# Optimization experiments

Measured on AMD Instinct MI355X. Metric: run time of the kernel, lower is better.

The kernel has to match this reference:

```python
import jax, jax.numpy as jnp
import numpy as np

C = 512
H = 8

def setup_inputs() -> dict:
    key = jax.random.key(0)
    ks = jax.random.split(key, 5)
    x = jax.random.normal(ks[0], (4, C, 2048), dtype=jnp.float32)
    # Conv1d(kernel_size=1) == pointwise linear: weight [out, in], bias [out]
    qkv_w = jax.random.normal(ks[1], (3 * C, C), dtype=jnp.float32) * (1.0 / np.sqrt(C))
    qkv_b = jax.random.normal(ks[2], (3 * C,), dtype=jnp.float32) * 0.02
    proj_w = jax.random.normal(ks[3], (C, C), dtype=jnp.float32) * (1.0 / np.sqrt(C))
    proj_b = jax.random.normal(ks[4], (C,), dtype=jnp.float32) * 0.02
    return {"x": x, "qkv_w": qkv_w, "qkv_b": qkv_b, "proj_w": proj_w, "proj_b": proj_b}

def reference(x, qkv_w, qkv_b, proj_w, proj_b):
    b, c, t = x.shape
    scale = c ** (-0.5)  # NOTE: full channel count, matching the torch module
    # pointwise conv: [3C, C] @ [b, C, T] -> [b, 3C, T]
    qkv = jnp.einsum('oc,bct->bot', qkv_w, x) + qkv_b[None, :, None]
    q, k, v = jnp.split(qkv, 3, axis=1)
    d = c // H
    q = q.reshape(b, H, d, t)
    k = k.reshape(b, H, d, t)
    v = v.reshape(b, H, d, t)
    attn = jnp.einsum('bhct,bhcs->bhts', q, k) * scale
    attn = jax.nn.softmax(attn, axis=-1)
    out = jnp.einsum('bhts,bhcs->bhct', attn, v)
    out = out.reshape(b, c, t)
    out = jnp.einsum('oc,bct->bot', proj_w, out) + proj_b[None, :, None]
    return x + out
```

## Files before the change

kernel.cpp:

```cpp
#include <hip/hip_runtime.h>
#include <hip/hip_bf16.h>
#include <math.h>

#define B_DIM 4
#define C_DIM 512
#define T_DIM 2048
#define H_DIM 8
#define OC3   1536
#define VN_STRIDE 2064
#define SCALE 0.044194173824159216f
#define SCALE2 (0.044194173824159216f * 1.4426950408889634f)

typedef unsigned short ushortT;
typedef unsigned int uintT;
typedef __attribute__((ext_vector_type(8))) short bf16x8;
typedef __attribute__((ext_vector_type(4))) short bf16x4;
typedef __attribute__((ext_vector_type(4))) float f32x4;

__device__ __forceinline__ ushortT f2bf(float f) {
    union { float f; uintT u; } v; v.f = f;
    uintT r = v.u + 0x7FFF + ((v.u >> 16) & 1);
    return (ushortT)(r >> 16);
}
__device__ __forceinline__ float bf2f(ushortT h) {
    union { uintT u; float f; } v; v.u = ((uintT)h) << 16;
    return v.f;
}
__device__ __forceinline__ uintT pack2bf(float a, float b) {
    uintT ua = __float_as_uint(a) + 0x8000u;
    uintT ub = __float_as_uint(b) + 0x8000u;
    return (ua >> 16) | (ub & 0xFFFF0000u);
}
__device__ __forceinline__ uintT cvtpk2bf(float a, float b) {
    union { __bf16 v[2]; uintT u; } c;
    c.v[0] = (__bf16)a; c.v[1] = (__bf16)b;
    return c.u;
}
__device__ __forceinline__ void gload_lds16(const ushortT* g, ushortT* l) {
    __builtin_amdgcn_global_load_lds(
        (const __attribute__((address_space(1))) void*)g,
        (__attribute__((address_space(3))) void*)l, 16, 0, 0);
}

__global__ __launch_bounds__(256) void prep(const float* __restrict__ x,
                                            const float* __restrict__ qw,
                                            const float* __restrict__ pw,
                                            ushortT* __restrict__ xb,
                                            ushortT* __restrict__ qwb,
                                            ushortT* __restrict__ pwb) {
    __shared__ float xs[64][65];
    const int tid = threadIdx.x;
    const int blk = blockIdx.x;
    if (blk >= 1024) {
        int idx = ((blk - 1024) * 256 + tid) * 4;
        if (idx < OC3 * C_DIM) {
            float4 v = *(const float4*)(qw + idx);
            qwb[idx + 0] = f2bf(v.x); qwb[idx + 1] = f2bf(v.y);
            qwb[idx + 2] = f2bf(v.z); qwb[idx + 3] = f2bf(v.w);
        } else {
            idx -= OC3 * C_DIM;
            float4 v = *(const float4*)(pw + idx);
            pwb[idx + 0] = f2bf(v.x); pwb[idx + 1] = f2bf(v.y);
            pwb[idx + 2] = f2bf(v.z); pwb[idx + 3] = f2bf(v.w);
        }
        return;
    }
    const int b = blk >> 8, rem = blk & 255;
    const int c0 = (rem >> 5) * 64, t0 = (rem & 31) * 64;
    #pragma unroll
    for (int it = 0; it < 4; ++it) {
        int idx = it * 256 + tid;
        int r = idx >> 4, ch = idx & 15;
        float4 v = *(const float4*)(x + ((size_t)(b * C_DIM + c0 + r)) * T_DIM + t0 + ch * 4);
        xs[r][ch * 4 + 0] = v.x; xs[r][ch * 4 + 1] = v.y;
        xs[r][ch * 4 + 2] = v.z; xs[r][ch * 4 + 3] = v.w;
    }
    __syncthreads();
    #pragma unroll
    for (int it = 0; it < 2; ++it) {
        int idx = it * 256 + tid;
        int rt = idx >> 3, ch = idx & 7;
        union { ushortT s[8]; uint4 v; } tmp;
        #pragma unroll
        for (int k = 0; k < 8; ++k) tmp.s[k] = f2bf(xs[ch * 8 + k][rt]);
        *(uint4*)(xb + ((size_t)b * T_DIM + t0 + rt) * C_DIM + c0 + ch * 8) = tmp.v;
    }
}

__global__ __launch_bounds__(256, 3) void gemm_qkv(const ushortT* __restrict__ A,
                                                   const ushortT* __restrict__ Bw,
                                                   const float* __restrict__ bias,
                                                   ushortT* __restrict__ out,
                                                   ushortT* __restrict__ Vn) {
    __shared__ __align__(16) ushortT As[8192], Bs[8192];
    const int tid = threadIdx.x, lane = tid & 63, wid = tid >> 6;
    const int u = lane & 15, q = lane >> 4;
    const int wm = wid & 1, wn = wid >> 1;
    const int m0 = blockIdx.x * 128, n0 = blockIdx.y * 128;
    const int lrow = lane >> 2, lcol = (lane & 3) * 8;

    f32x4 acc[4][4];
    const f32x4 z = {0.f, 0.f, 0.f, 0.f};
    #pragma unroll
    for (int mi = 0; mi < 4; ++mi)
        #pragma unroll
        for (int ni = 0; ni < 4; ++ni) acc[mi][ni] = z;

    for (int k0 = 0; k0 < 512; k0 += 64) {
        __syncthreads();
        gload_lds16(A  + (size_t)(m0 + wid * 32 +      lrow) * 512 + k0      + lcol, &As[(wid * 32     ) * 32]);
        gload_lds16(A  + (size_t)(m0 + wid * 32 + 16 + lrow) * 512 + k0      + lcol, &As[(wid * 32 + 16) * 32]);
        gload_lds16(A  + (size_t)(m0 + wid * 32 +      lrow) * 512 + k0 + 32 + lcol, &As[4096 + (wid * 32     ) * 32]);
        gload_lds16(A  + (size_t)(m0 + wid * 32 + 16 + lrow) * 512 + k0 + 32 + lcol, &As[4096 + (wid * 32 + 16) * 32]);
        gload_lds16(Bw + (size_t)(n0 + wid * 32 +      lrow) * 512 + k0      + lcol, &Bs[(wid * 32     ) * 32]);
        gload_lds16(Bw + (size_t)(n0 + wid * 32 + 16 + lrow) * 512 + k0      + lcol, &Bs[(wid * 32 + 16) * 32]);
        gload_lds16(Bw + (size_t)(n0 + wid * 32 +      lrow) * 512 + k0 + 32 + lcol, &Bs[4096 + (wid * 32     ) * 32]);
        gload_lds16(Bw + (size_t)(n0 + wid * 32 + 16 + lrow) * 512 + k0 + 32 + lcol, &Bs[4096 + (wid * 32 + 16) * 32]);
        __syncthreads();
        bf16x8 af[4][2], bfr[4][2];
        #pragma unroll
        for (int mi = 0; mi < 4; ++mi) {
            af[mi][0] = *(const bf16x8*)&As[(wm * 64 + mi * 16 + u) * 32 + q * 8];
            af[mi][1] = *(const bf16x8*)&As[4096 + (wm * 64 + mi * 16 + u) * 32 + q * 8];
        }
        #pragma unroll
        for (int ni = 0; ni < 4; ++ni) {
            bfr[ni][0] = *(const bf16x8*)&Bs[(wn * 64 + ni * 16 + u) * 32 + q * 8];
            bfr[ni][1] = *(const bf16x8*)&Bs[4096 + (wn * 64 + ni * 16 + u) * 32 + q * 8];
        }
        #pragma unroll
        for (int mi = 0; mi < 4; ++mi)
            #pragma unroll
            for (int ni = 0; ni < 4; ++ni) {
                acc[mi][ni] = __builtin_amdgcn_mfma_f32_16x16x32_bf16(
                    af[mi][0], bfr[ni][0], acc[mi][ni], 0, 0, 0);
                acc[mi][ni] = __builtin_amdgcn_mfma_f32_16x16x32_bf16(
                    af[mi][1], bfr[ni][1], acc[mi][ni], 0, 0, 0);
            }
    }
    if (n0 < 1024) {
        const float scl = (n0 < 512) ? SCALE2 : 1.0f;
        #pragma unroll
        for (int ni = 0; ni < 4; ++ni) {
            int o = n0 + wn * 64 + ni * 16 + u;
            float bv = bias[o];
            #pragma unroll
            for (int mi = 0; mi < 4; ++mi)
                #pragma unroll
                for (int r = 0; r < 4; ++r) {
                    int m = m0 + wm * 64 + mi * 16 + q * 4 + r;
                    out[(size_t)m * OC3 + o] = f2bf((acc[mi][ni][r] + bv) * scl);
                }
        }
    } else {
        #pragma unroll
        for (int ni = 0; ni < 4; ++ni) {
            int o = n0 + wn * 64 + ni * 16 + u;
            float bv = bias[o];
            int oo = o - 1024;
            int hv = oo >> 6, d = oo & 63;
            #pragma unroll
            for (int mi = 0; mi < 4; ++mi) {
                int m = m0 + wm * 64 + mi * 16 + q * 4;
                int b = m >> 11, t = m & 2047;
                uint2 w;
                w.x = pack2bf(acc[mi][ni][0] + bv, acc[mi][ni][1] + bv);
                w.y = pack2bf(acc[mi][ni][2] + bv, acc[mi][ni][3] + bv);
                *(uint2*)(Vn + ((size_t)((b * 8 + hv) * 64 + d)) * VN_STRIDE + t) = w;
            }
        }
    }
}

__global__ __launch_bounds__(256, 4)
void flash(const ushortT* __restrict__ qkvT, const ushortT* __restrict__ Vn,
           ushortT* __restrict__ AO)
{
    __shared__ __align__(16) ushortT smem[16384];

    const int tid = threadIdx.x, lane = tid & 63, wid = tid >> 6;
    const int u = lane & 15, q = lane >> 4;
    const int g = blockIdx.x;
    const int bh = (g & 7) * 4 + ((g >> 3) & 3);
    const int qt = g >> 5;
    const int bb = bh >> 3, h = bh & 7;
    const int q0 = qt * 64;
    const size_t qbase = (size_t)bb * T_DIM * OC3;

    bf16x8 qb[2];
    #pragma unroll
    for (int kst = 0; kst < 2; ++kst)
        qb[kst] = *(const bf16x8*)(qkvT + qbase
            + (size_t)(q0 + wid * 16 + u) * OC3 + h * 64 + kst * 32 + q * 8);

    const int rs = wid * 8 + (lane >> 3);
    const int sg = (lane & 7) ^ (rs & 7);
    const ushortT* ks0 = qkvT + qbase + (size_t)(rs     ) * OC3 + 512 + h * 64 + sg * 8;
    const ushortT* ks1 = qkvT + qbase + (size_t)(rs + 32) * OC3 + 512 + h * 64 + sg * 8;
    const ushortT* vs0 = Vn + ((size_t)bh * 64 + rs     ) * VN_STRIDE + sg * 8;
    const ushortT* vs1 = Vn + ((size_t)bh * 64 + rs + 32) * VN_STRIDE + sg * 8;

    f32x4 acc[4];
    const f32x4 z = {0.f, 0.f, 0.f, 0.f};
    #pragma unroll
    for (int ci = 0; ci < 4; ++ci) acc[ci] = z;
    f32x4 lacc = z;
    const bf16x4 ones = {(short)0x3F80, (short)0x3F80, (short)0x3F80, (short)0x3F80};

    gload_lds16(ks0, &smem[       wid * 512]);
    gload_lds16(ks1, &smem[2048 + wid * 512]);
    gload_lds16(vs0, &smem[8192 +        wid * 512]);
    gload_lds16(vs1, &smem[8192 + 2048 + wid * 512]);
    ks0 += 64 * OC3; ks1 += 64 * OC3; vs0 += 64; vs1 += 64;
    __syncthreads();

    int cur = 0;
    for (int rnd = 0; rnd < 32; ++rnd) {
        if (rnd < 31) {
            int nb = cur ^ 1;
            gload_lds16(ks0, &smem[nb * 4096 +        wid * 512]);
            gload_lds16(ks1, &smem[nb * 4096 + 2048 + wid * 512]);
            gload_lds16(vs0, &smem[8192 + nb * 4096 +        wid * 512]);
            gload_lds16(vs1, &smem[8192 + nb * 4096 + 2048 + wid * 512]);
            ks0 += 64 * OC3; ks1 += 64 * OC3; vs0 += 64; vs1 += 64;
        }
        const ushortT* Kb = &smem[cur * 4096];
        const ushortT* Vb = &smem[8192 + cur * 4096];
        bf16x8 ka[4][2];
        #pragma unroll
        for (int si = 0; si < 4; ++si)
            #pragma unroll
            for (int kst = 0; kst < 2; ++kst)
                ka[si][kst] = *(const bf16x8*)&Kb[(si * 16 + u) * 64
                    + (((kst * 4 + q) ^ (u & 7)) * 8)];
        bf16x4 va[4][4];
        #pragma unroll
        for (int si = 0; si < 4; ++si)
            #pragma unroll
            for (int ci = 0; ci < 4; ++ci)
                va[si][ci] = *(const bf16x4*)&Vb[(ci * 16 + u) * 64
                    + (((si * 2 + (q >> 1)) ^ (u & 7)) * 8) + (q & 1) * 4];

        #pragma unroll
        for (int si = 0; si < 4; ++si) {
            f32x4 sacc = z;
            sacc = __builtin_amdgcn_mfma_f32_16x16x32_bf16(
                ka[si][0], qb[0], sacc, 0, 0, 0);
            sacc = __builtin_amdgcn_mfma_f32_16x16x32_bf16(
                ka[si][1], qb[1], sacc, 0, 0, 0);
            float p0 = __builtin_amdgcn_exp2f(sacc[0]);
            float p1 = __builtin_amdgcn_exp2f(sacc[1]);
            float p2 = __builtin_amdgcn_exp2f(sacc[2]);
            float p3 = __builtin_amdgcn_exp2f(sacc[3]);
            union { uint2 u2; bf16x4 v; } pw;
            pw.u2.x = cvtpk2bf(p0, p1);
            pw.u2.y = cvtpk2bf(p2, p3);
            lacc = __builtin_amdgcn_mfma_f32_16x16x16bf16_1k(
                ones, pw.v, lacc, 0, 0, 0);
            #pragma unroll
            for (int ci = 0; ci < 4; ++ci)
                acc[ci] = __builtin_amdgcn_mfma_f32_16x16x16bf16_1k(
                    va[si][ci], pw.v, acc[ci], 0, 0, 0);
        }
        __syncthreads();
        cur ^= 1;
    }

    ushortT* Ob = smem + wid * 1152;
    float* Lb = (float*)(smem + 8192);
    if (q == 0) Lb[wid * 16 + u] = lacc[0];
    #pragma unroll
    for (int ci = 0; ci < 4; ++ci) {
        uint2 w;
        w.x = pack2bf(acc[ci][0], acc[ci][1]);
        w.y = pack2bf(acc[ci][2], acc[ci][3]);
        *(uint2*)&Ob[u * 72 + ci * 16 + q * 4] = w;
    }
    __syncthreads();
    {
        const int row = tid >> 2, cs = (tid & 3) * 16;
        const int w = row >> 4, r16 = row & 15;
        float linv = 1.0f / Lb[row];
        const ushortT* rp = smem + w * 1152 + r16 * 72 + cs;
        size_t orow = ((size_t)bb * T_DIM + q0 + row) * C_DIM + h * 64 + cs;
        #pragma unroll
        for (int j = 0; j < 2; ++j) {
            uint4 rv = *(const uint4*)(rp + j * 8);
            const uintT* rpp = (const uintT*)&rv;
            uint4 o;
            uintT* op = (uintT*)&o;
            #pragma unroll
            for (int k = 0; k < 4; ++k)
                op[k] = pack2bf(bf2f((ushortT)(rpp[k] & 0xFFFF)) * linv,
                                bf2f((ushortT)(rpp[k] >> 16)) * linv);
            *(uint4*)(AO + orow + j * 8) = o;
        }
    }
}

__global__ __launch_bounds__(256, 2) void gemm_proj(const ushortT* __restrict__ Wp,
                                                    const ushortT* __restrict__ AOv,
                                                    const float* __restrict__ bias,
                                                    const float* __restrict__ xres,
                                                    float* __restrict__ out) {
    __shared__ __align__(16) ushortT As[8192], Bs[4096];
    const int tid = threadIdx.x, lane = tid & 63, wid = tid >> 6;
    const int u = lane & 15, q = lane >> 4;
    const int wm = wid & 1, wn = wid >> 1;
    const int m0 = blockIdx.y * 128, n0 = blockIdx.x * 64;
    const int lrow = lane >> 2, lcol = (lane & 3) * 8;

    f32x4 acc[4][2];
    const f32x4 z = {0.f, 0.f, 0.f, 0.f};
    #pragma unroll
    for (int mi = 0; mi < 4; ++mi)
        #pragma unroll
        for (int ni = 0; ni < 2; ++ni) acc[mi][ni] = z;

    for (int k0 = 0; k0 < 512; k0 += 64) {
        __syncthreads();
        gload_lds16(Wp  + (size_t)(m0 + wid * 32 +      lrow) * 512 + k0      + lcol, &As[(wid * 32     ) * 32]);
        gload_lds16(Wp  + (size_t)(m0 + wid * 32 + 16 + lrow) * 512 + k0      + lcol, &As[(wid * 32 + 16) * 32]);
        gload_lds16(Wp  + (size_t)(m0 + wid * 32 +      lrow) * 512 + k0 + 32 + lcol, &As[4096 + (wid * 32     ) * 32]);
        gload_lds16(Wp  + (size_t)(m0 + wid * 32 + 16 + lrow) * 512 + k0 + 32 + lcol, &As[4096 + (wid * 32 + 16) * 32]);
        gload_lds16(AOv + (size_t)(n0 + wid * 16 + lrow) * 512 + k0      + lcol, &Bs[(wid * 16) * 32]);
        gload_lds16(AOv + (size_t)(n0 + wid * 16 + lrow) * 512 + k0 + 32 + lcol, &Bs[2048 + (wid * 16) * 32]);
        __syncthreads();
        bf16x8 af[4][2], bfr[2][2];
        #pragma unroll
        for (int mi = 0; mi < 4; ++mi) {
            af[mi][0] = *(const bf16x8*)&As[(wm * 64 + mi * 16 + u) * 32 + q * 8];
            af[mi][1] = *(const bf16x8*)&As[4096 + (wm * 64 + mi * 16 + u) * 32 + q * 8];
        }
        #pragma unroll
        for (int ni = 0; ni < 2; ++ni) {
            bfr[ni][0] = *(const bf16x8*)&Bs[(wn * 32 + ni * 16 + u) * 32 + q * 8];
            bfr[ni][1] = *(const bf16x8*)&Bs[2048 + (wn * 32 + ni * 16 + u) * 32 + q * 8];
        }
        #pragma unroll
        for (int mi = 0; mi < 4; ++mi)
            #pragma unroll
            for (int ni = 0; ni < 2; ++ni) {
                acc[mi][ni] = __builtin_amdgcn_mfma_f32_16x16x32_bf16(
                    af[mi][0], bfr[ni][0], acc[mi][ni], 0, 0, 0);
                acc[mi][ni] = __builtin_amdgcn_mfma_f32_16x16x32_bf16(
                    af[mi][1], bfr[ni][1], acc[mi][ni], 0, 0, 0);
            }
    }
    #pragma unroll
    for (int mi = 0; mi < 4; ++mi)
        #pragma unroll
        for (int r = 0; r < 4; ++r) {
            int o = m0 + wm * 64 + mi * 16 + q * 4 + r;
            float bv = bias[o];
            #pragma unroll
            for (int ni = 0; ni < 2; ++ni) {
                int n = n0 + wn * 32 + ni * 16 + u;
                int b = n >> 11, t = n & 2047;
                size_t oi = ((size_t)b * C_DIM + o) * T_DIM + t;
                out[oi] = acc[mi][ni][r] + bv + xres[oi];
            }
        }
}

extern "C" void kernel_launch(void* const* d_in, const int* in_sizes, int n_in,
                              void* d_out, int out_size, void* d_ws, size_t ws_size,
                              hipStream_t stream)
{
    const float* x      = (const float*)d_in[0];
    const float* qkv_w  = (const float*)d_in[1];
    const float* qkv_b  = (const float*)d_in[2];
    const float* proj_w = (const float*)d_in[3];
    const float* proj_b = (const float*)d_in[4];
    float* out = (float*)d_out;

    char* ws = (char*)d_ws;
    ushortT* xb   = (ushortT*)(ws);
    ushortT* wqb  = (ushortT*)(ws +  8388608);
    ushortT* wpb  = (ushortT*)(ws +  9961472);
    ushortT* qkvT = (ushortT*)(ws + 10485760);
    ushortT* Vn   = (ushortT*)(ws + 35651584);
    ushortT* AO   = (ushortT*)(ws + 44105728);

    prep     <<<2048, 256, 0, stream>>>(x, qkv_w, proj_w, xb, wqb, wpb);
    gemm_qkv <<<dim3(64, 12),   256, 0, stream>>>(xb, wqb, qkv_b, qkvT, Vn);
    flash    <<<1024,           256, 0, stream>>>(qkvT, Vn, AO);
    gemm_proj<<<dim3(128, 4),   256, 0, stream>>>(wpb, AO, proj_b, x, out);
}
```

Baseline: 158.9 us.

## Split flash attention key tiles across waves and reduce partials in LDS

```diff
diff --git a/kernel.cpp b/kernel.cpp
--- a/kernel.cpp
+++ b/kernel.cpp
@@ -176,7 +176,7 @@
 void flash(const ushortT* __restrict__ qkvT, const ushortT* __restrict__ Vn,
            ushortT* __restrict__ AO)
 {
-    __shared__ __align__(16) ushortT smem[16384];
+    __shared__ __align__(16) ushortT smem[18944];
 
     const int tid = threadIdx.x, lane = tid & 63, wid = tid >> 6;
     const int u = lane & 15, q = lane >> 4;
@@ -187,11 +187,13 @@
     const int q0 = qt * 64;
     const size_t qbase = (size_t)bb * T_DIM * OC3;
 
-    bf16x8 qb[2];
-    #pragma unroll
-    for (int kst = 0; kst < 2; ++kst)
-        qb[kst] = *(const bf16x8*)(qkvT + qbase
-            + (size_t)(q0 + wid * 16 + u) * OC3 + h * 64 + kst * 32 + q * 8);
+    bf16x8 qb[4][2];
+    #pragma unroll
+    for (int ti = 0; ti < 4; ++ti)
+        #pragma unroll
+        for (int kst = 0; kst < 2; ++kst)
+            qb[ti][kst] = *(const bf16x8*)(qkvT + qbase
+                + (size_t)(q0 + ti * 16 + u) * OC3 + h * 64 + kst * 32 + q * 8);
 
     const int rs = wid * 8 + (lane >> 3);
     const int sg = (lane & 7) ^ (rs & 7);
@@ -200,12 +202,13 @@
     const ushortT* vs0 = Vn + ((size_t)bh * 64 + rs     ) * VN_STRIDE + sg * 8;
     const ushortT* vs1 = Vn + ((size_t)bh * 64 + rs + 32) * VN_STRIDE + sg * 8;
 
-    f32x4 acc[4];
+    f32x4 acc[4][4];
     const f32x4 z = {0.f, 0.f, 0.f, 0.f};
     #pragma unroll
-    for (int ci = 0; ci < 4; ++ci) acc[ci] = z;
-    f32x4 lacc = z;
-    const bf16x4 ones = {(short)0x3F80, (short)0x3F80, (short)0x3F80, (short)0x3F80};
+    for (int ci = 0; ci < 4; ++ci)
+        #pragma unroll
+        for (int ti = 0; ti < 4; ++ti) acc[ci][ti] = z;
+    float lpart[4] = {0.f, 0.f, 0.f, 0.f};
 
     gload_lds16(ks0, &smem[       wid * 512]);
     gload_lds16(ks1, &smem[2048 + wid * 512]);
@@ -226,75 +229,94 @@
         }
         const ushortT* Kb = &smem[cur * 4096];
         const ushortT* Vb = &smem[8192 + cur * 4096];
-        bf16x8 ka[4][2];
-        #pragma unroll
-        for (int si = 0; si < 4; ++si)
-            #pragma unroll
-            for (int kst = 0; kst < 2; ++kst)
-                ka[si][kst] = *(const bf16x8*)&Kb[(si * 16 + u) * 64
-                    + (((kst * 4 + q) ^ (u & 7)) * 8)];
-        bf16x4 va[4][4];
-        #pragma unroll
-        for (int si = 0; si < 4; ++si)
-            #pragma unroll
-            for (int ci = 0; ci < 4; ++ci)
-                va[si][ci] = *(const bf16x4*)&Vb[(ci * 16 + u) * 64
-                    + (((si * 2 + (q >> 1)) ^ (u & 7)) * 8) + (q & 1) * 4];
-
-        #pragma unroll
-        for (int si = 0; si < 4; ++si) {
+        bf16x8 ka[2];
+        #pragma unroll
+        for (int kst = 0; kst < 2; ++kst)
+            ka[kst] = *(const bf16x8*)&Kb[(wid * 16 + u) * 64
+                + (((kst * 4 + q) ^ (u & 7)) * 8)];
+        bf16x4 va[4];
+        #pragma unroll
+        for (int ci = 0; ci < 4; ++ci)
+            va[ci] = *(const bf16x4*)&Vb[(ci * 16 + u) * 64
+                + (((wid * 2 + (q >> 1)) ^ (u & 7)) * 8) + (q & 1) * 4];
+
+        #pragma unroll
+        for (int ti = 0; ti < 4; ++ti) {
             f32x4 sacc = z;
             sacc = __builtin_amdgcn_mfma_f32_16x16x32_bf16(
-                ka[si][0], qb[0], sacc, 0, 0, 0);
+                ka[0], qb[ti][0], sacc, 0, 0, 0);
             sacc = __builtin_amdgcn_mfma_f32_16x16x32_bf16(
-                ka[si][1], qb[1], sacc, 0, 0, 0);
+                ka[1], qb[ti][1], sacc, 0, 0, 0);
             float p0 = __builtin_amdgcn_exp2f(sacc[0]);
             float p1 = __builtin_amdgcn_exp2f(sacc[1]);
             float p2 = __builtin_amdgcn_exp2f(sacc[2]);
             float p3 = __builtin_amdgcn_exp2f(sacc[3]);
+            lpart[ti] += (p0 + p1) + (p2 + p3);
             union { uint2 u2; bf16x4 v; } pw;
             pw.u2.x = cvtpk2bf(p0, p1);
             pw.u2.y = cvtpk2bf(p2, p3);
-            lacc = __builtin_amdgcn_mfma_f32_16x16x16bf16_1k(
-                ones, pw.v, lacc, 0, 0, 0);
             #pragma unroll
             for (int ci = 0; ci < 4; ++ci)
-                acc[ci] = __builtin_amdgcn_mfma_f32_16x16x16bf16_1k(
-                    va[si][ci], pw.v, acc[ci], 0, 0, 0);
+                acc[ci][ti] = __builtin_amdgcn_mfma_f32_16x16x16bf16_1k(
+                    va[ci], pw.v, acc[ci][ti], 0, 0, 0);
         }
         __syncthreads();
         cur ^= 1;
     }
 
-    ushortT* Ob = smem + wid * 1152;
-    float* Lb = (float*)(smem + 8192);
-    if (q == 0) Lb[wid * 16 + u] = lacc[0];
-    #pragma unroll
-    for (int ci = 0; ci < 4; ++ci) {
-        uint2 w;
-        w.x = pack2bf(acc[ci][0], acc[ci][1]);
-        w.y = pack2bf(acc[ci][2], acc[ci][3]);
-        *(uint2*)&Ob[u * 72 + ci * 16 + q * 4] = w;
-    }
+    #pragma unroll
+    for (int ti = 0; ti < 4; ++ti) {
+        float l = lpart[ti];
+        l += __shfl_xor(l, 16);
+        l += __shfl_xor(l, 32);
+        lpart[ti] = l;
+    }
+    ushortT* Ob = smem + wid * 4608;
+    float* Lb = (float*)(smem + 18432);
+    if (q == 0) {
+        #pragma unroll
+        for (int ti = 0; ti < 4; ++ti) Lb[wid * 64 + ti * 16 + u] = lpart[ti];
+    }
+    #pragma unroll
+    for (int ci = 0; ci < 4; ++ci)
+        #pragma unroll
+        for (int ti = 0; ti < 4; ++ti) {
+            uint2 w;
+            w.x = pack2bf(acc[ci][ti][0], acc[ci][ti][1]);
+            w.y = pack2bf(acc[ci][ti][2], acc[ci][ti][3]);
+            *(uint2*)&Ob[(ti * 16 + u) * 72 + ci * 16 + q * 4] = w;
+        }
     __syncthreads();
     {
-        const int row = tid >> 2, cs = (tid & 3) * 16;
-        const int w = row >> 4, r16 = row & 15;
-        float linv = 1.0f / Lb[row];
-        const ushortT* rp = smem + w * 1152 + r16 * 72 + cs;
-        size_t orow = ((size_t)bb * T_DIM + q0 + row) * C_DIM + h * 64 + cs;
-        #pragma unroll
-        for (int j = 0; j < 2; ++j) {
-            uint4 rv = *(const uint4*)(rp + j * 8);
-            const uintT* rpp = (const uintT*)&rv;
-            uint4 o;
-            uintT* op = (uintT*)&o;
-            #pragma unroll
-            for (int k = 0; k < 4; ++k)
-                op[k] = pack2bf(bf2f((ushortT)(rpp[k] & 0xFFFF)) * linv,
-                                bf2f((ushortT)(rpp[k] >> 16)) * linv);
-            *(uint4*)(AO + orow + j * 8) = o;
-        }
+        const int t = tid >> 2, cs = (tid & 3) * 16;
+        float linv = 1.0f / (Lb[t] + Lb[64 + t] + Lb[128 + t] + Lb[192 + t]);
+        float vs[16];
+        #pragma unroll
+        for (int j = 0; j < 16; ++j) vs[j] = 0.f;
+        #pragma unroll
+        for (int w = 0; w < 4; ++w) {
+            const ushortT* row = smem + w * 4608 + t * 72 + cs;
+            #pragma unroll
+            for (int j2 = 0; j2 < 2; ++j2) {
+                uint4 rv = *(const uint4*)(row + j2 * 8);
+                const uintT* rp = (const uintT*)&rv;
+                #pragma unroll
+                for (int k = 0; k < 4; ++k) {
+                    vs[j2 * 8 + k * 2 + 0] += bf2f((ushortT)(rp[k] & 0xFFFF));
+                    vs[j2 * 8 + k * 2 + 1] += bf2f((ushortT)(rp[k] >> 16));
+                }
+            }
+        }
+        uint4 o0, o1;
+        uintT* op0 = (uintT*)&o0; uintT* op1 = (uintT*)&o1;
+        #pragma unroll
+        for (int k = 0; k < 4; ++k) {
+            op0[k] = pack2bf(vs[k * 2] * linv, vs[k * 2 + 1] * linv);
+            op1[k] = pack2bf(vs[8 + k * 2] * linv, vs[8 + k * 2 + 1] * linv);
+        }
+        size_t orow = ((size_t)bb * T_DIM + q0 + t) * C_DIM + h * 64 + cs;
+        *(uint4*)(AO + orow) = o0;
+        *(uint4*)(AO + orow + 8) = o1;
     }
 }
 
```

Result: slower. 199.7 us (+25.7%).
